# Optimization experiments

Hardware: AMD Instinct MI355X
Metric: run time of the kernel (lower is better)

## Reference

```python
import jax, jax.numpy as jnp
import numpy as np

A_DIM, V_DIM, L_DIM, H = 512, 768, 1024, 512
B, S = 16, 2048


def setup_inputs() -> dict:
    key = jax.random.key(0)
    ks = jax.random.split(key, 20)
    w = lambda k, shp: jax.random.normal(k, shp, dtype=jnp.float32) * 0.02
    return {
        "a_input": jax.random.normal(ks[0], (B, S, A_DIM), dtype=jnp.float32),
        "v_input": jax.random.normal(ks[1], (B, S, V_DIM), dtype=jnp.float32),
        "l_input": jax.random.normal(ks[2], (B, S, L_DIM), dtype=jnp.float32),
        "h0": jax.random.normal(ks[3], (1, B, H), dtype=jnp.float32),
        "c0": jax.random.normal(ks[4], (1, B, H), dtype=jnp.float32),
        # 1x1 Conv1d == per-timestep Linear: weight [H, in_dim], bias [H]
        "Wa": w(ks[5], (H, A_DIM)), "ba": w(ks[6], (H,)),
        "Wv": w(ks[7], (H, V_DIM)), "bv": w(ks[8], (H,)),
        "Wl": w(ks[9], (H, L_DIM)), "bl": w(ks[10], (H,)),
        "Wc": w(ks[11], (H, 3 * H)), "bc": w(ks[12], (H,)),
        # LSTM params, PyTorch gate order (i, f, g, o)
        "Wih": w(ks[13], (4 * H, H)), "Whh": w(ks[14], (4 * H, H)),
        "bih": w(ks[15], (4 * H,)), "bhh": w(ks[16], (4 * H,)),
    }


def _lstm(x, h0, c0, Wih, Whh, bih, bhh):
    # x: [B, S, H]; h0/c0: [B, H]
    def step(carry, xt):
        h, c = carry
        gates = xt @ Wih.T + bih + h @ Whh.T + bhh  # [B, 4H]
        i, f, g, o = jnp.split(gates, 4, axis=-1)
        c = jax.nn.sigmoid(f) * c + jax.nn.sigmoid(i) * jnp.tanh(g)
        h = jax.nn.sigmoid(o) * jnp.tanh(c)
        return (h, c), h
    (hT, cT), hs = jax.lax.scan(step, (h0, c0), x.transpose(1, 0, 2))
    return hs.transpose(1, 0, 2), hT, cT  # [B,S,H], [B,H], [B,H]


def reference(a_input, v_input, l_input, h0, c0, Wa, ba, Wv, bv, Wl, bl,
              Wc, bc, Wih, Whh, bih, bhh):
    # 1x1 conv projections -> [B, S, H]
    a = a_input @ Wa.T + ba
    v = v_input @ Wv.T + bv
    l = l_input @ Wl.T + bl
    # attention fusion
    context = jnp.tanh(jnp.concatenate([a, v, l], axis=-1) @ Wc.T + bc)  # [B,S,H]
    scores = jnp.stack([
        jnp.sum(a * context, axis=-1),
        jnp.sum(v * context, axis=-1),
        jnp.sum(l * context, axis=-1),
    ], axis=-1)  # [B, S, 3]
    weight = jax.nn.softmax(scores, axis=-1)[..., None]  # [B,S,3,1]
    data = jnp.stack([a, v, l], axis=-2)  # [B,S,3,H]
    fusion = jnp.sum(data * weight, axis=-2)  # [B,S,H]
    r_out, hT, cT = _lstm(fusion, h0[0], c0[0], Wih, Whh, bih, bhh)
    return r_out, hT[None], cT[None]
```

## Files before the change

### kernel.cpp

```cpp
#include <hip/hip_runtime.h>
#include <stdint.h>

#define B_ 16
#define S_ 2048
#define H_ 512
#define M_ (B_ * S_)

template <int ACT>
__global__ __launch_bounds__(256) void gemm_xwt(
    const float* __restrict__ X, const float* __restrict__ W,
    const float* __restrict__ b1, const float* __restrict__ b2,
    float* __restrict__ Y, int K, int ldy)
{
  __shared__ float As[16][132];
  __shared__ float Bs[16][132];
  const int tid = threadIdx.x;
  const int bm = blockIdx.x, bn = blockIdx.y;
  const int ty = tid >> 4, tx = tid & 15;
  const int lr = tid >> 2, lk = (tid & 3) << 2;
  const float* Xb = X + (size_t)(bm * 128) * K;
  const float* Wb = W + (size_t)(bn * 128) * K;

  float acc[8][8] = {};

  for (int k0 = 0; k0 < K; k0 += 16) {
    float4 xa0 = *(const float4*)(Xb + (size_t)lr * K + k0 + lk);
    float4 xa1 = *(const float4*)(Xb + (size_t)(lr + 64) * K + k0 + lk);
    float4 wa0 = *(const float4*)(Wb + (size_t)lr * K + k0 + lk);
    float4 wa1 = *(const float4*)(Wb + (size_t)(lr + 64) * K + k0 + lk);
    __syncthreads();
    As[lk + 0][lr] = xa0.x; As[lk + 1][lr] = xa0.y; As[lk + 2][lr] = xa0.z; As[lk + 3][lr] = xa0.w;
    As[lk + 0][lr + 64] = xa1.x; As[lk + 1][lr + 64] = xa1.y; As[lk + 2][lr + 64] = xa1.z; As[lk + 3][lr + 64] = xa1.w;
    Bs[lk + 0][lr] = wa0.x; Bs[lk + 1][lr] = wa0.y; Bs[lk + 2][lr] = wa0.z; Bs[lk + 3][lr] = wa0.w;
    Bs[lk + 0][lr + 64] = wa1.x; Bs[lk + 1][lr + 64] = wa1.y; Bs[lk + 2][lr + 64] = wa1.z; Bs[lk + 3][lr + 64] = wa1.w;
    __syncthreads();
#pragma unroll
    for (int kk = 0; kk < 16; ++kk) {
      float4 a0 = *(const float4*)&As[kk][ty * 8];
      float4 a1 = *(const float4*)&As[kk][ty * 8 + 4];
      float4 b0 = *(const float4*)&Bs[kk][tx * 8];
      float4 b1v = *(const float4*)&Bs[kk][tx * 8 + 4];
      float av[8] = {a0.x, a0.y, a0.z, a0.w, a1.x, a1.y, a1.z, a1.w};
      float bv[8] = {b0.x, b0.y, b0.z, b0.w, b1v.x, b1v.y, b1v.z, b1v.w};
#pragma unroll
      for (int i = 0; i < 8; ++i)
#pragma unroll
        for (int j = 0; j < 8; ++j) acc[i][j] += av[i] * bv[j];
    }
  }

  const int ncol0 = bn * 128 + tx * 8;
  float bias[8];
#pragma unroll
  for (int j = 0; j < 8; ++j) {
    float bb = b1[ncol0 + j];
    if (b2) bb += b2[ncol0 + j];
    bias[j] = bb;
  }
#pragma unroll
  for (int i = 0; i < 8; ++i) {
    size_t row = (size_t)bm * 128 + ty * 8 + i;
    float* yp = Y + row * (size_t)ldy + ncol0;
    float out[8];
#pragma unroll
    for (int j = 0; j < 8; ++j) {
      float v = acc[i][j] + bias[j];
      if (ACT) v = tanhf(v);
      out[j] = v;
    }
    *(float4*)(yp)     = make_float4(out[0], out[1], out[2], out[3]);
    *(float4*)(yp + 4) = make_float4(out[4], out[5], out[6], out[7]);
  }
}

__global__ __launch_bounds__(256) void fusion_kernel(
    const float* __restrict__ F,
    const float* __restrict__ CTX,
    float* __restrict__ FU)
{
  const int row = blockIdx.x * 4 + (threadIdx.x >> 6);
  const int lane = threadIdx.x & 63;
  const float* a = F + (size_t)row * 1536;
  const float* v = a + 512;
  const float* l = a + 1024;
  const float* c = CTX + (size_t)row * 512;
  float sa = 0.f, sv = 0.f, sl = 0.f;
  for (int k = lane; k < 512; k += 64) {
    float cv = c[k];
    sa += a[k] * cv; sv += v[k] * cv; sl += l[k] * cv;
  }
#pragma unroll
  for (int off = 1; off < 64; off <<= 1) {
    sa += __shfl_xor(sa, off);
    sv += __shfl_xor(sv, off);
    sl += __shfl_xor(sl, off);
  }
  float m = fmaxf(sa, fmaxf(sv, sl));
  float ea = expf(sa - m), ev = expf(sv - m), el = expf(sl - m);
  float inv = 1.0f / (ea + ev + el);
  float wa = ea * inv, wv = ev * inv, wl = el * inv;
  float* fu = FU + (size_t)row * 512;
  for (int k = lane; k < 512; k += 64)
    fu[k] = wa * a[k] + wv * v[k] + wl * l[k];
}

__global__ __launch_bounds__(256, 1) void lstm_kernel(
    const float* __restrict__ G,
    const float* __restrict__ Whh,
    const float* __restrict__ h0,
    const float* __restrict__ c0,
    unsigned long long* __restrict__ ring,
    float* __restrict__ r_out,
    float* __restrict__ hT,
    float* __restrict__ cT)
{
  const int bi = blockIdx.x;
  const int b  = ((bi & 7) << 1) | ((bi >> 3) & 1);
  const int wg = bi >> 4;
  const int k0h = wg << 5;
  const int tid = threadIdx.x;

  __shared__ float h_lds[512];
  __shared__ float gates_lds[128];
  __shared__ float c_lds[32];

  const int col = tid >> 1;
  const int khalf = tid & 1;
  const int kbase = khalf << 8;
  const int g = col >> 5, ul = col & 31;
  const int gcol = g * 512 + k0h + ul;

  float4 warr[64];
  const float* wsrc = Whh + (size_t)gcol * 512 + kbase;
#pragma unroll
  for (int j = 0; j < 64; ++j) warr[j] = *(const float4*)(wsrc + j * 4);

  if (tid < 32) c_lds[tid] = c0[b * H_ + k0h + tid];
  __syncthreads();

  const float* gbase = G + (size_t)b * S_ * 2048;

  for (int t = 0; t < S_; ++t) {
    float gval = 0.f;
    if (khalf == 0) gval = gbase[(size_t)t * 2048 + gcol];

    if (t > 0) {
      const unsigned int want = (unsigned int)(t - 1);
      const unsigned long long* slot =
          ring + ((size_t)((t - 1) & 3) * B_ + b) * H_;
      unsigned long long v0, v1;
      do {
        v0 = __hip_atomic_load(slot + tid, __ATOMIC_RELAXED,
                               __HIP_MEMORY_SCOPE_AGENT);
      } while ((unsigned int)(v0 >> 32) != want);
      do {
        v1 = __hip_atomic_load(slot + tid + 256, __ATOMIC_RELAXED,
                               __HIP_MEMORY_SCOPE_AGENT);
      } while ((unsigned int)(v1 >> 32) != want);
      h_lds[tid]       = __builtin_bit_cast(float, (unsigned int)v0);
      h_lds[tid + 256] = __builtin_bit_cast(float, (unsigned int)v1);
    } else {
      const float* hsrc = h0 + b * H_;
      h_lds[tid] = hsrc[tid];
      h_lds[tid + 256] = hsrc[tid + 256];
    }
    __syncthreads();

    float4 s4 = make_float4(0.f, 0.f, 0.f, 0.f);
#pragma unroll
    for (int j = 0; j < 64; ++j) {
      float4 hv = *(const float4*)&h_lds[kbase + (j << 2)];
      s4.x += warr[j].x * hv.x;
      s4.y += warr[j].y * hv.y;
      s4.z += warr[j].z * hv.z;
      s4.w += warr[j].w * hv.w;
    }
    float sum = (s4.x + s4.y) + (s4.z + s4.w);
    sum += __shfl_xor(sum, 1);
    if (khalf == 0) gates_lds[col] = sum + gval;
    __syncthreads();

    if (tid < 32) {
      const int u = tid;
      float ip = gates_lds[u], fp = gates_lds[32 + u];
      float gp = gates_lds[64 + u], op = gates_lds[96 + u];
      float ig = 1.f / (1.f + expf(-ip));
      float fg = 1.f / (1.f + expf(-fp));
      float gg = tanhf(gp);
      float og = 1.f / (1.f + expf(-op));
      float cn = fg * c_lds[u] + ig * gg;
      c_lds[u] = cn;
      float hn = og * tanhf(cn);
      unsigned long long pk =
          ((unsigned long long)(unsigned int)t << 32) |
          (unsigned long long)__builtin_bit_cast(unsigned int, hn);
      __hip_atomic_store(ring + ((size_t)(t & 3) * B_ + b) * H_ + k0h + u,
                         pk, __ATOMIC_RELAXED, __HIP_MEMORY_SCOPE_AGENT);
      r_out[((size_t)b * S_ + t) * H_ + k0h + u] = hn;
      if (t == S_ - 1) {
        hT[b * H_ + k0h + u] = hn;
        cT[b * H_ + k0h + u] = cn;
      }
    }
    __syncthreads();
  }
}

extern "C" void kernel_launch(void* const* d_in, const int* in_sizes, int n_in,
                              void* d_out, int out_size, void* d_ws, size_t ws_size,
                              hipStream_t stream)
{
  const float* a_in = (const float*)d_in[0];
  const float* v_in = (const float*)d_in[1];
  const float* l_in = (const float*)d_in[2];
  const float* h0   = (const float*)d_in[3];
  const float* c0   = (const float*)d_in[4];
  const float* Wa = (const float*)d_in[5];   const float* ba = (const float*)d_in[6];
  const float* Wv = (const float*)d_in[7];   const float* bv = (const float*)d_in[8];
  const float* Wl = (const float*)d_in[9];   const float* bl = (const float*)d_in[10];
  const float* Wc = (const float*)d_in[11];  const float* bc = (const float*)d_in[12];
  const float* Wih = (const float*)d_in[13]; const float* Whh = (const float*)d_in[14];
  const float* bih = (const float*)d_in[15]; const float* bhh = (const float*)d_in[16];

  char* ws = (char*)d_ws;
  float* Fbuf = (float*)ws;
  float* Gbuf = (float*)ws;
  float* CTX  = (float*)(ws + 268435456ull);
  float* FU   = (float*)(ws + 335544320ull);
  unsigned long long* ringp = (unsigned long long*)(ws + 402653184ull);

  dim3 blk(256);
  gemm_xwt<0><<<dim3(256, 4), blk, 0, stream>>>(a_in, Wa, ba, nullptr, Fbuf + 0,    512,  1536);
  gemm_xwt<0><<<dim3(256, 4), blk, 0, stream>>>(v_in, Wv, bv, nullptr, Fbuf + 512,  768,  1536);
  gemm_xwt<0><<<dim3(256, 4), blk, 0, stream>>>(l_in, Wl, bl, nullptr, Fbuf + 1024, 1024, 1536);
  gemm_xwt<1><<<dim3(256, 4), blk, 0, stream>>>(Fbuf, Wc, bc, nullptr, CTX, 1536, 512);
  fusion_kernel<<<dim3(8192), blk, 0, stream>>>(Fbuf, CTX, FU);
  gemm_xwt<0><<<dim3(256, 16), blk, 0, stream>>>(FU, Wih, bih, bhh, Gbuf, 512, 2048);
  float* out = (float*)d_out;
  lstm_kernel<<<dim3(256), blk, 0, stream>>>(Gbuf, Whh, h0, c0, ringp,
                                             out, out + 16777216ull,
                                             out + 16777216ull + 8192ull);
}
```

Measured before the change: 10.78 ms.

## Exchange raw gate pre-activations and compute all hidden units redundantly per block

Each LSTM block now publishes its partial gate sums (tagged with the timestep) to a global ring instead of publishing finished hidden values. Every block polls all 2048 gate values for its batch row and redundantly computes the full 512-wide cell update, with each thread owning two units. This removes two of the three __syncthreads per step and the single-warp activation bottleneck, and the next step's input gates are prefetched. In exchange, each block does more polling traffic and redundant activation math, and the ring layout changes to 2 slots of 2048 entries, which needs enough workspace.

```diff
diff --git a/kernel.cpp b/kernel.cpp
--- a/kernel.cpp
+++ b/kernel.cpp
@@ -104,6 +104,11 @@
     fu[k] = wa * a[k] + wv * v[k] + wl * l[k];
 }
 
+__device__ __forceinline__ float sigf(float x) { return 1.f / (1.f + expf(-x)); }
+__device__ __forceinline__ float lo32f(unsigned long long w) {
+  return __builtin_bit_cast(float, (unsigned int)w);
+}
+
 __global__ __launch_bounds__(256, 1) void lstm_kernel(
     const float* __restrict__ G,
     const float* __restrict__ Whh,
@@ -120,9 +125,7 @@
   const int k0h = wg << 5;
   const int tid = threadIdx.x;
 
-  __shared__ float h_lds[512];
-  __shared__ float gates_lds[128];
-  __shared__ float c_lds[32];
+  __shared__ float h_lds[2][512];
 
   const int col = tid >> 1;
   const int khalf = tid & 1;
@@ -135,41 +138,27 @@
 #pragma unroll
   for (int j = 0; j < 64; ++j) warr[j] = *(const float4*)(wsrc + j * 4);
 
-  if (tid < 32) c_lds[tid] = c0[b * H_ + k0h + tid];
+  const int u0 = tid << 1;
+  const float* Gb = G + (size_t)b * S_ * 2048;
+  const bool writer = ((tid >> 4) == wg);
+
+  h_lds[0][tid]       = h0[b * H_ + tid];
+  h_lds[0][tid + 256] = h0[b * H_ + tid + 256];
+  float c_a = c0[b * H_ + u0];
+  float c_b = c0[b * H_ + u0 + 1];
+  float2 gv_i = *(const float2*)(Gb + u0);
+  float2 gv_f = *(const float2*)(Gb + 512 + u0);
+  float2 gv_g = *(const float2*)(Gb + 1024 + u0);
+  float2 gv_o = *(const float2*)(Gb + 1536 + u0);
   __syncthreads();
 
-  const float* gbase = G + (size_t)b * S_ * 2048;
-
+  int buf = 0;
   for (int t = 0; t < S_; ++t) {
-    float gval = 0.f;
-    if (khalf == 0) gval = gbase[(size_t)t * 2048 + gcol];
-
-    if (t > 0) {
-      const unsigned int want = (unsigned int)(t - 1);
-      const unsigned long long* slot =
-          ring + ((size_t)((t - 1) & 3) * B_ + b) * H_;
-      unsigned long long v0, v1;
-      do {
-        v0 = __hip_atomic_load(slot + tid, __ATOMIC_RELAXED,
-                               __HIP_MEMORY_SCOPE_AGENT);
-      } while ((unsigned int)(v0 >> 32) != want);
-      do {
-        v1 = __hip_atomic_load(slot + tid + 256, __ATOMIC_RELAXED,
-                               __HIP_MEMORY_SCOPE_AGENT);
-      } while ((unsigned int)(v1 >> 32) != want);
-      h_lds[tid]       = __builtin_bit_cast(float, (unsigned int)v0);
-      h_lds[tid + 256] = __builtin_bit_cast(float, (unsigned int)v1);
-    } else {
-      const float* hsrc = h0 + b * H_;
-      h_lds[tid] = hsrc[tid];
-      h_lds[tid + 256] = hsrc[tid + 256];
-    }
-    __syncthreads();
-
+    const float* hb = &h_lds[buf][kbase];
     float4 s4 = make_float4(0.f, 0.f, 0.f, 0.f);
 #pragma unroll
     for (int j = 0; j < 64; ++j) {
-      float4 hv = *(const float4*)&h_lds[kbase + (j << 2)];
+      float4 hv = *(const float4*)(hb + (j << 2));
       s4.x += warr[j].x * hv.x;
       s4.y += warr[j].y * hv.y;
       s4.z += warr[j].z * hv.z;
@@ -177,32 +166,67 @@
     }
     float sum = (s4.x + s4.y) + (s4.z + s4.w);
     sum += __shfl_xor(sum, 1);
-    if (khalf == 0) gates_lds[col] = sum + gval;
-    __syncthreads();
-
-    if (tid < 32) {
-      const int u = tid;
-      float ip = gates_lds[u], fp = gates_lds[32 + u];
-      float gp = gates_lds[64 + u], op = gates_lds[96 + u];
-      float ig = 1.f / (1.f + expf(-ip));
-      float fg = 1.f / (1.f + expf(-fp));
-      float gg = tanhf(gp);
-      float og = 1.f / (1.f + expf(-op));
-      float cn = fg * c_lds[u] + ig * gg;
-      c_lds[u] = cn;
-      float hn = og * tanhf(cn);
+
+    unsigned long long* slot = ring + ((size_t)((t & 1) * B_ + b)) * 2048;
+    if (khalf == 0) {
       unsigned long long pk =
           ((unsigned long long)(unsigned int)t << 32) |
-          (unsigned long long)__builtin_bit_cast(unsigned int, hn);
-      __hip_atomic_store(ring + ((size_t)(t & 3) * B_ + b) * H_ + k0h + u,
-                         pk, __ATOMIC_RELAXED, __HIP_MEMORY_SCOPE_AGENT);
-      r_out[((size_t)b * S_ + t) * H_ + k0h + u] = hn;
+          (unsigned long long)__builtin_bit_cast(unsigned int, sum);
+      __hip_atomic_store(slot + gcol, pk, __ATOMIC_RELAXED,
+                         __HIP_MEMORY_SCOPE_AGENT);
+    }
+
+    const unsigned long long* sp = slot + u0;
+    const unsigned int want = (unsigned int)t;
+    unsigned long long wi0, wi1, wf0, wf1, wg0, wg1, wo0, wo1;
+    for (;;) {
+      wi0 = __hip_atomic_load(sp + 0,    __ATOMIC_RELAXED, __HIP_MEMORY_SCOPE_AGENT);
+      wi1 = __hip_atomic_load(sp + 1,    __ATOMIC_RELAXED, __HIP_MEMORY_SCOPE_AGENT);
+      wf0 = __hip_atomic_load(sp + 512,  __ATOMIC_RELAXED, __HIP_MEMORY_SCOPE_AGENT);
+      wf1 = __hip_atomic_load(sp + 513,  __ATOMIC_RELAXED, __HIP_MEMORY_SCOPE_AGENT);
+      wg0 = __hip_atomic_load(sp + 1024, __ATOMIC_RELAXED, __HIP_MEMORY_SCOPE_AGENT);
+      wg1 = __hip_atomic_load(sp + 1025, __ATOMIC_RELAXED, __HIP_MEMORY_SCOPE_AGENT);
+      wo0 = __hip_atomic_load(sp + 1536, __ATOMIC_RELAXED, __HIP_MEMORY_SCOPE_AGENT);
+      wo1 = __hip_atomic_load(sp + 1537, __ATOMIC_RELAXED, __HIP_MEMORY_SCOPE_AGENT);
+      unsigned int bad =
+          ((unsigned int)(wi0 >> 32) ^ want) | ((unsigned int)(wi1 >> 32) ^ want) |
+          ((unsigned int)(wf0 >> 32) ^ want) | ((unsigned int)(wf1 >> 32) ^ want) |
+          ((unsigned int)(wg0 >> 32) ^ want) | ((unsigned int)(wg1 >> 32) ^ want) |
+          ((unsigned int)(wo0 >> 32) ^ want) | ((unsigned int)(wo1 >> 32) ^ want);
+      if (bad == 0) break;
+    }
+
+    float Gi0 = gv_i.x, Gi1 = gv_i.y, Gf0 = gv_f.x, Gf1 = gv_f.y;
+    float Gg0 = gv_g.x, Gg1 = gv_g.y, Go0 = gv_o.x, Go1 = gv_o.y;
+    if (t + 1 < S_) {
+      const float* gn = Gb + (size_t)(t + 1) * 2048 + u0;
+      gv_i = *(const float2*)(gn);
+      gv_f = *(const float2*)(gn + 512);
+      gv_g = *(const float2*)(gn + 1024);
+      gv_o = *(const float2*)(gn + 1536);
+    }
+
+    float i0 = lo32f(wi0) + Gi0, i1 = lo32f(wi1) + Gi1;
+    float f0 = lo32f(wf0) + Gf0, f1 = lo32f(wf1) + Gf1;
+    float g0 = lo32f(wg0) + Gg0, g1 = lo32f(wg1) + Gg1;
+    float o0 = lo32f(wo0) + Go0, o1 = lo32f(wo1) + Go1;
+
+    float cA = sigf(f0) * c_a + sigf(i0) * tanhf(g0);
+    float cB = sigf(f1) * c_b + sigf(i1) * tanhf(g1);
+    c_a = cA; c_b = cB;
+    float hA = sigf(o0) * tanhf(cA);
+    float hB = sigf(o1) * tanhf(cB);
+
+    *(float2*)&h_lds[buf ^ 1][u0] = make_float2(hA, hB);
+    if (writer) {
+      *(float2*)(r_out + ((size_t)b * S_ + t) * H_ + u0) = make_float2(hA, hB);
       if (t == S_ - 1) {
-        hT[b * H_ + k0h + u] = hn;
-        cT[b * H_ + k0h + u] = cn;
+        *(float2*)(hT + b * H_ + u0) = make_float2(hA, hB);
+        *(float2*)(cT + b * H_ + u0) = make_float2(cA, cB);
       }
     }
     __syncthreads();
+    buf ^= 1;
   }
 }
 
```

After: 12.07 ms. 1.12x slower.

## Add per-step sent flags and double-buffered h to LSTM cross-block sync

Applied to the files above, without the earlier changes.

Restructures the persistent LSTM step loop. After producing its hidden slice, each block publishes a per-block 'sent' flag, and 16 threads poll the 16 producer flags before the whole block reads the ring data. That read now needs only a single combined check instead of two spinning loops per thread. The hidden state is double-buffered in LDS, and the next step's G input is prefetched during the wait, which removes one barrier per step. The cost is extra flag stores and loads, plus a fresh workspace region for flags that are not reset between launches, though the stale-value check uses the timestep tag.

```diff
diff --git a/kernel.cpp b/kernel.cpp
--- a/kernel.cpp
+++ b/kernel.cpp
@@ -104,12 +104,18 @@
     fu[k] = wa * a[k] + wv * v[k] + wl * l[k];
 }
 
+__device__ __forceinline__ float sigf(float x) { return 1.f / (1.f + expf(-x)); }
+__device__ __forceinline__ float lo32f(unsigned long long w) {
+  return __builtin_bit_cast(float, (unsigned int)w);
+}
+
 __global__ __launch_bounds__(256, 1) void lstm_kernel(
     const float* __restrict__ G,
     const float* __restrict__ Whh,
     const float* __restrict__ h0,
     const float* __restrict__ c0,
     unsigned long long* __restrict__ ring,
+    unsigned long long* __restrict__ sent,
     float* __restrict__ r_out,
     float* __restrict__ hT,
     float* __restrict__ cT)
@@ -120,7 +126,7 @@
   const int k0h = wg << 5;
   const int tid = threadIdx.x;
 
-  __shared__ float h_lds[512];
+  __shared__ float h_lds[2][512];
   __shared__ float gates_lds[128];
   __shared__ float c_lds[32];
 
@@ -135,41 +141,21 @@
 #pragma unroll
   for (int j = 0; j < 64; ++j) warr[j] = *(const float4*)(wsrc + j * 4);
 
+  const float* gbase = G + (size_t)b * S_ * 2048;
+
   if (tid < 32) c_lds[tid] = c0[b * H_ + k0h + tid];
+  h_lds[0][tid]       = h0[b * H_ + tid];
+  h_lds[0][tid + 256] = h0[b * H_ + tid + 256];
+  float gval = (khalf == 0) ? gbase[gcol] : 0.f;
   __syncthreads();
 
-  const float* gbase = G + (size_t)b * S_ * 2048;
-
+  int buf = 0;
   for (int t = 0; t < S_; ++t) {
-    float gval = 0.f;
-    if (khalf == 0) gval = gbase[(size_t)t * 2048 + gcol];
-
-    if (t > 0) {
-      const unsigned int want = (unsigned int)(t - 1);
-      const unsigned long long* slot =
-          ring + ((size_t)((t - 1) & 3) * B_ + b) * H_;
-      unsigned long long v0, v1;
-      do {
-        v0 = __hip_atomic_load(slot + tid, __ATOMIC_RELAXED,
-                               __HIP_MEMORY_SCOPE_AGENT);
-      } while ((unsigned int)(v0 >> 32) != want);
-      do {
-        v1 = __hip_atomic_load(slot + tid + 256, __ATOMIC_RELAXED,
-                               __HIP_MEMORY_SCOPE_AGENT);
-      } while ((unsigned int)(v1 >> 32) != want);
-      h_lds[tid]       = __builtin_bit_cast(float, (unsigned int)v0);
-      h_lds[tid + 256] = __builtin_bit_cast(float, (unsigned int)v1);
-    } else {
-      const float* hsrc = h0 + b * H_;
-      h_lds[tid] = hsrc[tid];
-      h_lds[tid + 256] = hsrc[tid + 256];
-    }
-    __syncthreads();
-
+    const float* hb = &h_lds[buf][kbase];
     float4 s4 = make_float4(0.f, 0.f, 0.f, 0.f);
 #pragma unroll
     for (int j = 0; j < 64; ++j) {
-      float4 hv = *(const float4*)&h_lds[kbase + (j << 2)];
+      float4 hv = *(const float4*)(hb + (j << 2));
       s4.x += warr[j].x * hv.x;
       s4.y += warr[j].y * hv.y;
       s4.z += warr[j].z * hv.z;
@@ -180,29 +166,65 @@
     if (khalf == 0) gates_lds[col] = sum + gval;
     __syncthreads();
 
+    unsigned long long* slot = ring + ((size_t)(t & 3) * B_ + b) * H_;
+
     if (tid < 32) {
       const int u = tid;
       float ip = gates_lds[u], fp = gates_lds[32 + u];
       float gp = gates_lds[64 + u], op = gates_lds[96 + u];
-      float ig = 1.f / (1.f + expf(-ip));
-      float fg = 1.f / (1.f + expf(-fp));
-      float gg = tanhf(gp);
-      float og = 1.f / (1.f + expf(-op));
+      float ig = sigf(ip), fg = sigf(fp);
+      float gg = tanhf(gp), og = sigf(op);
       float cn = fg * c_lds[u] + ig * gg;
       c_lds[u] = cn;
       float hn = og * tanhf(cn);
       unsigned long long pk =
           ((unsigned long long)(unsigned int)t << 32) |
           (unsigned long long)__builtin_bit_cast(unsigned int, hn);
-      __hip_atomic_store(ring + ((size_t)(t & 3) * B_ + b) * H_ + k0h + u,
-                         pk, __ATOMIC_RELAXED, __HIP_MEMORY_SCOPE_AGENT);
+      __hip_atomic_store(slot + k0h + u, pk, __ATOMIC_RELAXED,
+                         __HIP_MEMORY_SCOPE_AGENT);
+      if (u == 0) {
+        __hip_atomic_store(sent + ((size_t)(t & 3) * B_ + b) * 16 + wg,
+                           (unsigned long long)(unsigned int)t << 32,
+                           __ATOMIC_RELAXED, __HIP_MEMORY_SCOPE_AGENT);
+      }
       r_out[((size_t)b * S_ + t) * H_ + k0h + u] = hn;
       if (t == S_ - 1) {
         hT[b * H_ + k0h + u] = hn;
         cT[b * H_ + k0h + u] = cn;
       }
     }
-    __syncthreads();
+
+    if (t + 1 < S_) {
+      if (tid < 16) {
+        const unsigned long long* sp =
+            sent + ((size_t)(t & 3) * B_ + b) * 16 + tid;
+        unsigned int got;
+        do {
+          got = (unsigned int)(__hip_atomic_load(sp, __ATOMIC_RELAXED,
+                                                 __HIP_MEMORY_SCOPE_AGENT) >> 32);
+        } while (got != (unsigned int)t);
+      }
+      __syncthreads();
+
+      const unsigned int want = (unsigned int)t;
+      unsigned long long v0 = __hip_atomic_load(slot + tid, __ATOMIC_RELAXED,
+                                                __HIP_MEMORY_SCOPE_AGENT);
+      unsigned long long v1 = __hip_atomic_load(slot + tid + 256, __ATOMIC_RELAXED,
+                                                __HIP_MEMORY_SCOPE_AGENT);
+      while ((((unsigned int)(v0 >> 32)) ^ want) |
+             (((unsigned int)(v1 >> 32)) ^ want)) {
+        v0 = __hip_atomic_load(slot + tid, __ATOMIC_RELAXED,
+                               __HIP_MEMORY_SCOPE_AGENT);
+        v1 = __hip_atomic_load(slot + tid + 256, __ATOMIC_RELAXED,
+                               __HIP_MEMORY_SCOPE_AGENT);
+      }
+      h_lds[buf ^ 1][tid]       = lo32f(v0);
+      h_lds[buf ^ 1][tid + 256] = lo32f(v1);
+
+      if (khalf == 0) gval = gbase[(size_t)(t + 1) * 2048 + gcol];
+      __syncthreads();
+      buf ^= 1;
+    }
   }
 }
 
@@ -228,6 +250,7 @@
   float* CTX  = (float*)(ws + 268435456ull);
   float* FU   = (float*)(ws + 335544320ull);
   unsigned long long* ringp = (unsigned long long*)(ws + 402653184ull);
+  unsigned long long* sentp = (unsigned long long*)(ws + 402653184ull + 262144ull);
 
   dim3 blk(256);
   gemm_xwt<0><<<dim3(256, 4), blk, 0, stream>>>(a_in, Wa, ba, nullptr, Fbuf + 0,    512,  1536);
@@ -237,7 +260,7 @@
   fusion_kernel<<<dim3(8192), blk, 0, stream>>>(Fbuf, CTX, FU);
   gemm_xwt<0><<<dim3(256, 16), blk, 0, stream>>>(FU, Wih, bih, bhh, Gbuf, 512, 2048);
   float* out = (float*)d_out;
-  lstm_kernel<<<dim3(256), blk, 0, stream>>>(Gbuf, Whh, h0, c0, ringp,
+  lstm_kernel<<<dim3(256), blk, 0, stream>>>(Gbuf, Whh, h0, c0, ringp, sentp,
                                              out, out + 16777216ull,
                                              out + 16777216ull + 8192ull);
 }
```

Result: faster. 10.50 ms (-2.6%).
